# Kernel optimization log

Measured on AMD Instinct MI355X. Metric: run time of the kernel, lower is better.

## Reference

```python
import jax, jax.numpy as jnp
import numpy as np

B, T, C, H = 128, 512, 128, 64  # batch, seq, n_embd, head_size


def setup_inputs() -> dict:
    key = jax.random.key(0)
    ks = jax.random.split(key, 6)
    s = 1.0 / np.sqrt(C)
    return {
        "x": jax.random.normal(ks[0], (B, T, C), dtype=jnp.float32),
        "Wg": jax.random.normal(ks[1], (C, C), dtype=jnp.float32) * s,
        "bg": jnp.zeros((C,), dtype=jnp.float32),
        "Wk": jax.random.normal(ks[2], (C, H), dtype=jnp.float32) * s,
        "Wq": jax.random.normal(ks[3], (C, H), dtype=jnp.float32) * s,
        "Wv": jax.random.normal(ks[4], (C, H), dtype=jnp.float32) * s,
    }


def reference(x, Wg, bg, Wk, Wq, Wv):
    # GateLayer: x * sigmoid(Linear(x))
    g = jax.nn.sigmoid(jnp.einsum('btc,cd->btd', x, Wg) + bg)
    xg = x * g
    k = jnp.einsum('btc,ch->bth', xg, Wk)
    q = jnp.einsum('btc,ch->bth', xg, Wq)
    v = jnp.einsum('btc,ch->bth', xg, Wv)
    # NOTE: original scales by C**-0.5 (n_embd), not head_size**-0.5
    scale = C ** -0.5
    wei = jnp.einsum('bqh,bkh->bqk', q, k) * scale  # [B,T,T]
    causal = jnp.tril(jnp.ones((T, T), dtype=bool))
    wei = jnp.where(causal, wei, -jnp.inf)
    wei = jax.nn.softmax(wei, axis=-1)
    # dropout is identity in eval mode
    out = jnp.einsum('bqk,bkh->bqh', wei, v)  # [B,T,H]
    return out
```

## Files before the change

kernel.cpp:

```cpp
#include <hip/hip_runtime.h>


#define BB 128
#define TB 512
#define CC 128
#define HH 64

static constexpr float SCALE = 0.088388347648318447f;

typedef __attribute__((ext_vector_type(8))) short bf16x8;
typedef __attribute__((ext_vector_type(8))) unsigned short u16x8;
typedef __attribute__((ext_vector_type(4))) float f32x4;

__device__ inline unsigned short f2bf(float f) {
    union { float f; unsigned u; } x; x.f = f;
    unsigned r = x.u + 0x7fff + ((x.u >> 16) & 1);
    return (unsigned short)(r >> 16);
}
__device__ inline float bf2f(unsigned short h) {
    union { unsigned u; float f; } x; x.u = ((unsigned)h) << 16;
    return x.f;
}

__global__ void prep_weights(const float* __restrict__ Wg, const float* __restrict__ Wk,
                             const float* __restrict__ Wq, const float* __restrict__ Wv,
                             unsigned short* __restrict__ WgT, unsigned short* __restrict__ WkT,
                             unsigned short* __restrict__ WqT, unsigned short* __restrict__ WvT)
{
    int idx = blockIdx.x * 256 + threadIdx.x;
    if (idx < 16384) {
        int n = idx >> 7, k = idx & 127;
        WgT[idx] = f2bf(Wg[k * CC + n]);
    } else {
        int j = idx - 16384;
        int mtx = j >> 13;
        int r = j & 8191;
        int n = r >> 7, k = r & 127;
        const float* W = (mtx == 0) ? Wk : (mtx == 1) ? Wq : Wv;
        unsigned short* WT = (mtx == 0) ? WkT : (mtx == 1) ? WqT : WvT;
        WT[r] = f2bf(W[k * HH + n]);
    }
}

__global__ __launch_bounds__(256, 3) void gate_qkv_kernel(
    const float* __restrict__ x, const float* __restrict__ bg,
    const unsigned short* __restrict__ WgT, const unsigned short* __restrict__ WkT,
    const unsigned short* __restrict__ WqT, const unsigned short* __restrict__ WvT,
    unsigned short* __restrict__ qo, unsigned short* __restrict__ ko,
    unsigned short* __restrict__ vto)
{
    __shared__ unsigned short xsb[128 * 136];

    const int tid  = threadIdx.x;
    const int wv   = tid >> 6;
    const int lane = tid & 63;
    const int l15  = lane & 15;
    const int quad = lane >> 4;
    const int R0   = blockIdx.x * 128;

#pragma unroll
    for (int it = 0; it < 16; ++it) {
        int fid = tid + 256 * it;
        int r = fid >> 5, c4 = fid & 31;
        float4 xv = *(const float4*)(x + (size_t)(R0 + r) * CC + c4 * 4);
        ushort4 h;
        h.x = f2bf(xv.x); h.y = f2bf(xv.y); h.z = f2bf(xv.z); h.w = f2bf(xv.w);
        *(ushort4*)(xsb + r * 136 + c4 * 4) = h;
    }
    __syncthreads();

    bf16x8 bx[2][4];
#pragma unroll
    for (int mt = 0; mt < 2; ++mt)
#pragma unroll
        for (int kc = 0; kc < 4; ++kc)
            bx[mt][kc] = *(const bf16x8*)(xsb + (32 * wv + 16 * mt + l15) * 136 +
                                          kc * 32 + quad * 8);

    f32x4 acc[8][2];
#pragma unroll
    for (int nt = 0; nt < 8; ++nt)
#pragma unroll
        for (int mt = 0; mt < 2; ++mt) acc[nt][mt] = (f32x4){0.f, 0.f, 0.f, 0.f};

#pragma unroll
    for (int nt = 0; nt < 8; ++nt) {
        bf16x8 aw[4];
#pragma unroll
        for (int kc = 0; kc < 4; ++kc)
            aw[kc] = *(const bf16x8*)(WgT + (16 * nt + l15) * CC + kc * 32 + quad * 8);
#pragma unroll
        for (int mt = 0; mt < 2; ++mt)
#pragma unroll
            for (int kc = 0; kc < 4; ++kc)
                acc[nt][mt] = __builtin_amdgcn_mfma_f32_16x16x32_bf16(
                    aw[kc], bx[mt][kc], acc[nt][mt], 0, 0, 0);
    }

#pragma unroll
    for (int nt = 0; nt < 8; ++nt) {
        float4 bgv = *(const float4*)(bg + 16 * nt + quad * 4);
#pragma unroll
        for (int mt = 0; mt < 2; ++mt) {
            int m = 32 * wv + 16 * mt + l15;
            unsigned short* p = xsb + m * 136 + 16 * nt + quad * 4;
            ushort4 xb = *(const ushort4*)p;
            float e0 = __expf(-(acc[nt][mt][0] + bgv.x));
            float e1 = __expf(-(acc[nt][mt][1] + bgv.y));
            float e2 = __expf(-(acc[nt][mt][2] + bgv.z));
            float e3 = __expf(-(acc[nt][mt][3] + bgv.w));
            ushort4 o;
            o.x = f2bf(bf2f(xb.x) * __builtin_amdgcn_rcpf(1.f + e0));
            o.y = f2bf(bf2f(xb.y) * __builtin_amdgcn_rcpf(1.f + e1));
            o.z = f2bf(bf2f(xb.z) * __builtin_amdgcn_rcpf(1.f + e2));
            o.w = f2bf(bf2f(xb.w) * __builtin_amdgcn_rcpf(1.f + e3));
            *(ushort4*)p = o;
        }
    }
    __syncthreads();

#pragma unroll
    for (int mt = 0; mt < 2; ++mt)
#pragma unroll
        for (int kc = 0; kc < 4; ++kc)
            bx[mt][kc] = *(const bf16x8*)(xsb + (32 * wv + 16 * mt + l15) * 136 +
                                          kc * 32 + quad * 8);

    const int b = R0 >> 9, t0 = R0 & 511;
    for (int pj = 0; pj < 3; ++pj) {
        const unsigned short* WT = (pj == 0) ? WkT : (pj == 1) ? WqT : WvT;
        f32x4 pacc[4][2];
#pragma unroll
        for (int nt = 0; nt < 4; ++nt)
#pragma unroll
            for (int mt = 0; mt < 2; ++mt) pacc[nt][mt] = (f32x4){0.f, 0.f, 0.f, 0.f};

#pragma unroll
        for (int nt = 0; nt < 4; ++nt) {
            bf16x8 aw[4];
#pragma unroll
            for (int kc = 0; kc < 4; ++kc)
                aw[kc] = *(const bf16x8*)(WT + (16 * nt + l15) * CC + kc * 32 + quad * 8);
#pragma unroll
            for (int mt = 0; mt < 2; ++mt)
#pragma unroll
                for (int kc = 0; kc < 4; ++kc)
                    pacc[nt][mt] = __builtin_amdgcn_mfma_f32_16x16x32_bf16(
                        aw[kc], bx[mt][kc], pacc[nt][mt], 0, 0, 0);
        }

        if (pj < 2) {
            unsigned short* O = (pj == 0) ? ko : qo;
#pragma unroll
            for (int nt = 0; nt < 4; ++nt)
#pragma unroll
                for (int mt = 0; mt < 2; ++mt) {
                    int m = 32 * wv + 16 * mt + l15;
                    ushort4 h;
                    h.x = f2bf(pacc[nt][mt][0]); h.y = f2bf(pacc[nt][mt][1]);
                    h.z = f2bf(pacc[nt][mt][2]); h.w = f2bf(pacc[nt][mt][3]);
                    *(ushort4*)(O + (size_t)(R0 + m) * HH + 16 * nt + quad * 4) = h;
                }
        } else {
#pragma unroll
            for (int nt = 0; nt < 4; ++nt)
#pragma unroll
                for (int mt = 0; mt < 2; ++mt) {
                    int m = 32 * wv + 16 * mt + l15;
                    unsigned short* dst =
                        vto + (size_t)b * (HH * TB) + (16 * nt + quad * 4) * TB + t0 + m;
#pragma unroll
                    for (int r = 0; r < 4; ++r)
                        dst[r * TB] = f2bf(pacc[nt][mt][r]);
                }
        }
    }
}

__global__ __launch_bounds__(256) void attn_kernel(
    const unsigned short* __restrict__ q, const unsigned short* __restrict__ k,
    const unsigned short* __restrict__ vt, float* __restrict__ out)
{
    __shared__ unsigned short ks[64 * 72];
    __shared__ unsigned short vs[64 * 72];
    __shared__ unsigned short ps[64 * 76];

    const int tid  = threadIdx.x;
    const int wave = tid >> 6;
    const int lane = tid & 63;
    const int l15  = lane & 15;
    const int quad = lane >> 4;
    const int pr   = blockIdx.x;
    const int b    = blockIdx.y;
    const size_t base = (size_t)b * TB * HH;
    const int qtA = pr;

    const int r0 = tid >> 3,          c80 = (tid & 7) * 8;
    const int r1 = (tid + 256) >> 3,  c81 = (tid & 7) * 8;

    bf16x8 kr0 = *(const bf16x8*)(k + base + (size_t)r0 * HH + c80);
    bf16x8 kr1 = *(const bf16x8*)(k + base + (size_t)r1 * HH + c81);
    bf16x8 vr0 = *(const bf16x8*)(vt + base + (size_t)r0 * TB + c80);
    bf16x8 vr1 = *(const bf16x8*)(vt + base + (size_t)r1 * TB + c81);

    int qt = qtA, q0 = qtA * 64;
    const unsigned short* qrow = q + base + (size_t)(q0 + 16 * wave + l15) * HH;
    bf16x8 aq0 = *(const bf16x8*)(qrow + quad * 8);
    bf16x8 aq1 = *(const bf16x8*)(qrow + 32 + quad * 8);

    f32x4 o4[4];
    float mrow[4], lrow[4];
#pragma unroll
    for (int nt = 0; nt < 4; ++nt) o4[nt] = (f32x4){0.f, 0.f, 0.f, 0.f};
#pragma unroll
    for (int r = 0; r < 4; ++r) { mrow[r] = -1e30f; lrow[r] = 0.f; }

    for (int it = 0; it < 9; ++it) {
        const int kt = (it <= qtA) ? it : it - qtA - 1;

        __syncthreads();
        *(bf16x8*)(ks + r0 * 72 + c80) = kr0;
        *(bf16x8*)(ks + r1 * 72 + c81) = kr1;
        *(bf16x8*)(vs + r0 * 72 + c80) = vr0;
        *(bf16x8*)(vs + r1 * 72 + c81) = vr1;
        __syncthreads();

        if (it < 8) {
            const int itn = it + 1;
            const int ktn = (itn <= qtA) ? itn : itn - qtA - 1;
            const int k0n = ktn * 64;
            kr0 = *(const bf16x8*)(k + base + (size_t)(k0n + r0) * HH + c80);
            kr1 = *(const bf16x8*)(k + base + (size_t)(k0n + r1) * HH + c81);
            vr0 = *(const bf16x8*)(vt + base + (size_t)r0 * TB + k0n + c80);
            vr1 = *(const bf16x8*)(vt + base + (size_t)r1 * TB + k0n + c81);
        }

        f32x4 s[4];
#pragma unroll
        for (int nt = 0; nt < 4; ++nt) {
            bf16x8 bk0 = *(const bf16x8*)(ks + (16 * nt + l15) * 72 + quad * 8);
            bf16x8 bk1 = *(const bf16x8*)(ks + (16 * nt + l15) * 72 + 32 + quad * 8);
            f32x4 z = (f32x4){0.f, 0.f, 0.f, 0.f};
            z = __builtin_amdgcn_mfma_f32_16x16x32_bf16(aq0, bk0, z, 0, 0, 0);
            z = __builtin_amdgcn_mfma_f32_16x16x32_bf16(aq1, bk1, z, 0, 0, 0);
            s[nt] = z;
        }

        const bool diag = (kt == qt);
        float mx[4];
#pragma unroll
        for (int r = 0; r < 4; ++r) mx[r] = -1e30f;
#pragma unroll
        for (int nt = 0; nt < 4; ++nt)
#pragma unroll
            for (int r = 0; r < 4; ++r) {
                float sv = s[nt][r] * SCALE;
                if (diag && (16 * nt + l15) > (16 * wave + quad * 4 + r)) sv = -1e30f;
                s[nt][r] = sv;
                mx[r] = fmaxf(mx[r], sv);
            }

#pragma unroll
        for (int r = 0; r < 4; ++r) {
            mx[r] = fmaxf(mx[r], __shfl_xor(mx[r], 1));
            mx[r] = fmaxf(mx[r], __shfl_xor(mx[r], 2));
            mx[r] = fmaxf(mx[r], __shfl_xor(mx[r], 4));
            mx[r] = fmaxf(mx[r], __shfl_xor(mx[r], 8));
        }
        float alpha[4], psum[4];
#pragma unroll
        for (int r = 0; r < 4; ++r) {
            float mn = fmaxf(mrow[r], mx[r]);
            alpha[r] = __expf(mrow[r] - mn);
            mrow[r] = mn;
            psum[r] = 0.f;
        }
#pragma unroll
        for (int nt = 0; nt < 4; ++nt)
#pragma unroll
            for (int r = 0; r < 4; ++r) {
                float e = __expf(s[nt][r] - mrow[r]);
                psum[r] += e;
                ps[(16 * wave + quad * 4 + r) * 76 + 16 * nt + l15] = f2bf(e);
            }
#pragma unroll
        for (int r = 0; r < 4; ++r) {
            psum[r] += __shfl_xor(psum[r], 1);
            psum[r] += __shfl_xor(psum[r], 2);
            psum[r] += __shfl_xor(psum[r], 4);
            psum[r] += __shfl_xor(psum[r], 8);
            lrow[r] = lrow[r] * alpha[r] + psum[r];
        }
#pragma unroll
        for (int nt = 0; nt < 4; ++nt)
#pragma unroll
            for (int r = 0; r < 4; ++r) o4[nt][r] *= alpha[r];

        bf16x8 ap0 = *(const bf16x8*)(ps + (16 * wave + l15) * 76 + quad * 8);
        bf16x8 ap1 = *(const bf16x8*)(ps + (16 * wave + l15) * 76 + 32 + quad * 8);
#pragma unroll
        for (int nt = 0; nt < 4; ++nt) {
            bf16x8 bv0 = *(const bf16x8*)(vs + (16 * nt + l15) * 72 + quad * 8);
            bf16x8 bv1 = *(const bf16x8*)(vs + (16 * nt + l15) * 72 + 32 + quad * 8);
            o4[nt] = __builtin_amdgcn_mfma_f32_16x16x32_bf16(ap0, bv0, o4[nt], 0, 0, 0);
            o4[nt] = __builtin_amdgcn_mfma_f32_16x16x32_bf16(ap1, bv1, o4[nt], 0, 0, 0);
        }

        if (kt == qt) {
            float inv[4];
#pragma unroll
            for (int r = 0; r < 4; ++r) inv[r] = __builtin_amdgcn_rcpf(lrow[r]);
#pragma unroll
            for (int nt = 0; nt < 4; ++nt)
#pragma unroll
                for (int r = 0; r < 4; ++r)
                    out[base + (size_t)(q0 + 16 * wave + quad * 4 + r) * HH + 16 * nt + l15] =
                        o4[nt][r] * inv[r];
            if (it < 8) {
                qt = 7 - pr; q0 = qt * 64;
                const unsigned short* qrow2 = q + base + (size_t)(q0 + 16 * wave + l15) * HH;
                aq0 = *(const bf16x8*)(qrow2 + quad * 8);
                aq1 = *(const bf16x8*)(qrow2 + 32 + quad * 8);
#pragma unroll
                for (int nt = 0; nt < 4; ++nt) o4[nt] = (f32x4){0.f, 0.f, 0.f, 0.f};
#pragma unroll
                for (int r = 0; r < 4; ++r) { mrow[r] = -1e30f; lrow[r] = 0.f; }
            }
        }
    }
}

extern "C" void kernel_launch(void* const* d_in, const int* in_sizes, int n_in,
                              void* d_out, int out_size, void* d_ws, size_t ws_size,
                              hipStream_t stream) {
    const float* x  = (const float*)d_in[0];
    const float* Wg = (const float*)d_in[1];
    const float* bg = (const float*)d_in[2];
    const float* Wk = (const float*)d_in[3];
    const float* Wq = (const float*)d_in[4];
    const float* Wv = (const float*)d_in[5];
    float* out = (float*)d_out;

    unsigned short* ws = (unsigned short*)d_ws;
    const size_t BTH = (size_t)BB * TB * HH;
    unsigned short* qo  = ws;
    unsigned short* ko  = ws + BTH;
    unsigned short* vto = ws + 2 * BTH;
    unsigned short* WgT = ws + 3 * BTH;
    unsigned short* WkT = WgT + 16384;
    unsigned short* WqT = WkT + 8192;
    unsigned short* WvT = WqT + 8192;

    hipLaunchKernelGGL(prep_weights, dim3(160), dim3(256), 0, stream,
                       Wg, Wk, Wq, Wv, WgT, WkT, WqT, WvT);
    hipLaunchKernelGGL(gate_qkv_kernel, dim3(BB * TB / 128), dim3(256), 0, stream,
                       x, bg, WgT, WkT, WqT, WvT, qo, ko, vto);
    hipLaunchKernelGGL(attn_kernel, dim3(4, BB), dim3(256), 0, stream,
                       qo, ko, vto, out);
}
```

Measured before the change: 133.4 us.

## Share K/V tile loads across paired query tiles and prefetch weight fragments

The attention kernel now processes both paired query tiles (pr and 7-pr) at the same time. Each K/V tile is staged into shared memory once and used by both tiles, instead of the earlier sequential pass that reloaded the low tile's K/V range. The gate/QKV kernel double-buffers the weight fragment loads so the next n-tile's weights are fetched while the current MFMAs run, and the projection loop is fully unrolled. Launch bounds drop to 2 blocks per CU to give room for the extra registers from the dual accumulators, which risks lower occupancy.

```diff
diff --git a/kernel.cpp b/kernel.cpp
--- a/kernel.cpp
+++ b/kernel.cpp
@@ -42,7 +42,7 @@
     }
 }
 
-__global__ __launch_bounds__(256, 3) void gate_qkv_kernel(
+__global__ __launch_bounds__(256, 2) void gate_qkv_kernel(
     const float* __restrict__ x, const float* __restrict__ bg,
     const unsigned short* __restrict__ WgT, const unsigned short* __restrict__ WkT,
     const unsigned short* __restrict__ WqT, const unsigned short* __restrict__ WvT,
@@ -83,18 +83,30 @@
 #pragma unroll
         for (int mt = 0; mt < 2; ++mt) acc[nt][mt] = (f32x4){0.f, 0.f, 0.f, 0.f};
 
+    bf16x8 awA[4], awB[4];
+#pragma unroll
+    for (int kc = 0; kc < 4; ++kc)
+        awA[kc] = *(const bf16x8*)(WgT + l15 * CC + kc * 32 + quad * 8);
+
 #pragma unroll
     for (int nt = 0; nt < 8; ++nt) {
-        bf16x8 aw[4];
-#pragma unroll
-        for (int kc = 0; kc < 4; ++kc)
-            aw[kc] = *(const bf16x8*)(WgT + (16 * nt + l15) * CC + kc * 32 + quad * 8);
+        if (nt < 7) {
+#pragma unroll
+            for (int kc = 0; kc < 4; ++kc)
+                awB[kc] = *(const bf16x8*)(WgT + (16 * (nt + 1) + l15) * CC + kc * 32 + quad * 8);
+        } else {
+#pragma unroll
+            for (int kc = 0; kc < 4; ++kc)
+                awB[kc] = *(const bf16x8*)(WkT + l15 * CC + kc * 32 + quad * 8);
+        }
 #pragma unroll
         for (int mt = 0; mt < 2; ++mt)
 #pragma unroll
             for (int kc = 0; kc < 4; ++kc)
                 acc[nt][mt] = __builtin_amdgcn_mfma_f32_16x16x32_bf16(
-                    aw[kc], bx[mt][kc], acc[nt][mt], 0, 0, 0);
+                    awA[kc], bx[mt][kc], acc[nt][mt], 0, 0, 0);
+#pragma unroll
+        for (int kc = 0; kc < 4; ++kc) awA[kc] = awB[kc];
     }
 
 #pragma unroll
@@ -127,8 +139,8 @@
                                           kc * 32 + quad * 8);
 
     const int b = R0 >> 9, t0 = R0 & 511;
+#pragma unroll
     for (int pj = 0; pj < 3; ++pj) {
-        const unsigned short* WT = (pj == 0) ? WkT : (pj == 1) ? WqT : WvT;
         f32x4 pacc[4][2];
 #pragma unroll
         for (int nt = 0; nt < 4; ++nt)
@@ -137,16 +149,23 @@
 
 #pragma unroll
         for (int nt = 0; nt < 4; ++nt) {
-            bf16x8 aw[4];
-#pragma unroll
-            for (int kc = 0; kc < 4; ++kc)
-                aw[kc] = *(const bf16x8*)(WT + (16 * nt + l15) * CC + kc * 32 + quad * 8);
+            if (!(pj == 2 && nt == 3)) {
+                const unsigned short* Wcur = (pj == 0) ? WkT : (pj == 1) ? WqT : WvT;
+                const unsigned short* Wnxt = (pj == 0) ? WqT : WvT;
+                const unsigned short* Wp   = (nt < 3) ? Wcur : Wnxt;
+                const int ntn = (nt < 3) ? nt + 1 : 0;
+#pragma unroll
+                for (int kc = 0; kc < 4; ++kc)
+                    awB[kc] = *(const bf16x8*)(Wp + (16 * ntn + l15) * CC + kc * 32 + quad * 8);
+            }
 #pragma unroll
             for (int mt = 0; mt < 2; ++mt)
 #pragma unroll
                 for (int kc = 0; kc < 4; ++kc)
                     pacc[nt][mt] = __builtin_amdgcn_mfma_f32_16x16x32_bf16(
-                        aw[kc], bx[mt][kc], pacc[nt][mt], 0, 0, 0);
+                        awA[kc], bx[mt][kc], pacc[nt][mt], 0, 0, 0);
+#pragma unroll
+            for (int kc = 0; kc < 4; ++kc) awA[kc] = awB[kc];
         }
 
         if (pj < 2) {
@@ -177,7 +196,81 @@
     }
 }
 
-__global__ __launch_bounds__(256) void attn_kernel(
+__device__ __forceinline__ void smax_pv(f32x4* s, float* mrow, float* lrow,
+                                        f32x4* o4, unsigned short* ps,
+                                        const unsigned short* vs,
+                                        int wave, int l15, int quad)
+{
+    float mx[4];
+#pragma unroll
+    for (int r = 0; r < 4; ++r) mx[r] = -1e30f;
+#pragma unroll
+    for (int nt = 0; nt < 4; ++nt)
+#pragma unroll
+        for (int r = 0; r < 4; ++r) mx[r] = fmaxf(mx[r], s[nt][r]);
+#pragma unroll
+    for (int r = 0; r < 4; ++r) {
+        mx[r] = fmaxf(mx[r], __shfl_xor(mx[r], 1));
+        mx[r] = fmaxf(mx[r], __shfl_xor(mx[r], 2));
+        mx[r] = fmaxf(mx[r], __shfl_xor(mx[r], 4));
+        mx[r] = fmaxf(mx[r], __shfl_xor(mx[r], 8));
+    }
+    float alpha[4], psum[4];
+#pragma unroll
+    for (int r = 0; r < 4; ++r) {
+        float mn = fmaxf(mrow[r], mx[r]);
+        alpha[r] = __expf(mrow[r] - mn);
+        mrow[r] = mn;
+        psum[r] = 0.f;
+    }
+#pragma unroll
+    for (int nt = 0; nt < 4; ++nt)
+#pragma unroll
+        for (int r = 0; r < 4; ++r) {
+            float e = __expf(s[nt][r] - mrow[r]);
+            psum[r] += e;
+            ps[(16 * wave + quad * 4 + r) * 76 + 16 * nt + l15] = f2bf(e);
+        }
+#pragma unroll
+    for (int r = 0; r < 4; ++r) {
+        psum[r] += __shfl_xor(psum[r], 1);
+        psum[r] += __shfl_xor(psum[r], 2);
+        psum[r] += __shfl_xor(psum[r], 4);
+        psum[r] += __shfl_xor(psum[r], 8);
+        lrow[r] = lrow[r] * alpha[r] + psum[r];
+    }
+#pragma unroll
+    for (int nt = 0; nt < 4; ++nt)
+#pragma unroll
+        for (int r = 0; r < 4; ++r) o4[nt][r] *= alpha[r];
+
+    bf16x8 ap0 = *(const bf16x8*)(ps + (16 * wave + l15) * 76 + quad * 8);
+    bf16x8 ap1 = *(const bf16x8*)(ps + (16 * wave + l15) * 76 + 32 + quad * 8);
+#pragma unroll
+    for (int nt = 0; nt < 4; ++nt) {
+        bf16x8 bv0 = *(const bf16x8*)(vs + (16 * nt + l15) * 72 + quad * 8);
+        bf16x8 bv1 = *(const bf16x8*)(vs + (16 * nt + l15) * 72 + 32 + quad * 8);
+        o4[nt] = __builtin_amdgcn_mfma_f32_16x16x32_bf16(ap0, bv0, o4[nt], 0, 0, 0);
+        o4[nt] = __builtin_amdgcn_mfma_f32_16x16x32_bf16(ap1, bv1, o4[nt], 0, 0, 0);
+    }
+}
+
+__device__ __forceinline__ void attn_epilogue(const f32x4* o4, const float* lrow,
+                                              float* out, size_t base, int q0,
+                                              int wave, int l15, int quad)
+{
+    float inv[4];
+#pragma unroll
+    for (int r = 0; r < 4; ++r) inv[r] = __builtin_amdgcn_rcpf(lrow[r]);
+#pragma unroll
+    for (int nt = 0; nt < 4; ++nt)
+#pragma unroll
+        for (int r = 0; r < 4; ++r)
+            out[base + (size_t)(q0 + 16 * wave + quad * 4 + r) * HH + 16 * nt + l15] =
+                o4[nt][r] * inv[r];
+}
+
+__global__ __launch_bounds__(256, 2) void attn_kernel(
     const unsigned short* __restrict__ q, const unsigned short* __restrict__ k,
     const unsigned short* __restrict__ vt, float* __restrict__ out)
 {
@@ -193,141 +286,100 @@
     const int pr   = blockIdx.x;
     const int b    = blockIdx.y;
     const size_t base = (size_t)b * TB * HH;
-    const int qtA = pr;
-
-    const int r0 = tid >> 3,          c80 = (tid & 7) * 8;
-    const int r1 = (tid + 256) >> 3,  c81 = (tid & 7) * 8;
-
-    bf16x8 kr0 = *(const bf16x8*)(k + base + (size_t)r0 * HH + c80);
-    bf16x8 kr1 = *(const bf16x8*)(k + base + (size_t)r1 * HH + c81);
-    bf16x8 vr0 = *(const bf16x8*)(vt + base + (size_t)r0 * TB + c80);
-    bf16x8 vr1 = *(const bf16x8*)(vt + base + (size_t)r1 * TB + c81);
-
-    int qt = qtA, q0 = qtA * 64;
-    const unsigned short* qrow = q + base + (size_t)(q0 + 16 * wave + l15) * HH;
-    bf16x8 aq0 = *(const bf16x8*)(qrow + quad * 8);
-    bf16x8 aq1 = *(const bf16x8*)(qrow + 32 + quad * 8);
-
-    f32x4 o4[4];
-    float mrow[4], lrow[4];
-#pragma unroll
-    for (int nt = 0; nt < 4; ++nt) o4[nt] = (f32x4){0.f, 0.f, 0.f, 0.f};
-#pragma unroll
-    for (int r = 0; r < 4; ++r) { mrow[r] = -1e30f; lrow[r] = 0.f; }
-
-    for (int it = 0; it < 9; ++it) {
-        const int kt = (it <= qtA) ? it : it - qtA - 1;
-
+
+    const int qtA = pr, qtB = 7 - pr;
+    const int q0A = qtA * 64, q0B = qtB * 64;
+
+    const int r0 = tid >> 3, c8 = (tid & 7) * 8;
+    const int r1 = r0 + 32;
+
+    bf16x8 kr0 = *(const bf16x8*)(k + base + (size_t)r0 * HH + c8);
+    bf16x8 kr1 = *(const bf16x8*)(k + base + (size_t)r1 * HH + c8);
+    bf16x8 vr0 = *(const bf16x8*)(vt + base + (size_t)r0 * TB + c8);
+    bf16x8 vr1 = *(const bf16x8*)(vt + base + (size_t)r1 * TB + c8);
+
+    const unsigned short* qrA = q + base + (size_t)(q0A + 16 * wave + l15) * HH;
+    const unsigned short* qrB = q + base + (size_t)(q0B + 16 * wave + l15) * HH;
+    bf16x8 aqA0 = *(const bf16x8*)(qrA + quad * 8);
+    bf16x8 aqA1 = *(const bf16x8*)(qrA + 32 + quad * 8);
+    bf16x8 aqB0 = *(const bf16x8*)(qrB + quad * 8);
+    bf16x8 aqB1 = *(const bf16x8*)(qrB + 32 + quad * 8);
+
+    f32x4 oA[4], oB[4];
+    float mA[4], lA[4], mB[4], lB[4];
+#pragma unroll
+    for (int nt = 0; nt < 4; ++nt) {
+        oA[nt] = (f32x4){0.f, 0.f, 0.f, 0.f};
+        oB[nt] = (f32x4){0.f, 0.f, 0.f, 0.f};
+    }
+#pragma unroll
+    for (int r = 0; r < 4; ++r) { mA[r] = -1e30f; lA[r] = 0.f; mB[r] = -1e30f; lB[r] = 0.f; }
+
+    const int nIt = qtB + 1;
+    for (int kt = 0; kt < nIt; ++kt) {
         __syncthreads();
-        *(bf16x8*)(ks + r0 * 72 + c80) = kr0;
-        *(bf16x8*)(ks + r1 * 72 + c81) = kr1;
-        *(bf16x8*)(vs + r0 * 72 + c80) = vr0;
-        *(bf16x8*)(vs + r1 * 72 + c81) = vr1;
+        *(bf16x8*)(ks + r0 * 72 + c8) = kr0;
+        *(bf16x8*)(ks + r1 * 72 + c8) = kr1;
+        *(bf16x8*)(vs + r0 * 72 + c8) = vr0;
+        *(bf16x8*)(vs + r1 * 72 + c8) = vr1;
         __syncthreads();
 
-        if (it < 8) {
-            const int itn = it + 1;
-            const int ktn = (itn <= qtA) ? itn : itn - qtA - 1;
-            const int k0n = ktn * 64;
-            kr0 = *(const bf16x8*)(k + base + (size_t)(k0n + r0) * HH + c80);
-            kr1 = *(const bf16x8*)(k + base + (size_t)(k0n + r1) * HH + c81);
-            vr0 = *(const bf16x8*)(vt + base + (size_t)r0 * TB + k0n + c80);
-            vr1 = *(const bf16x8*)(vt + base + (size_t)r1 * TB + k0n + c81);
-        }
-
-        f32x4 s[4];
+        if (kt + 1 < nIt) {
+            const int k0n = (kt + 1) * 64;
+            kr0 = *(const bf16x8*)(k + base + (size_t)(k0n + r0) * HH + c8);
+            kr1 = *(const bf16x8*)(k + base + (size_t)(k0n + r1) * HH + c8);
+            vr0 = *(const bf16x8*)(vt + base + (size_t)r0 * TB + k0n + c8);
+            vr1 = *(const bf16x8*)(vt + base + (size_t)r1 * TB + k0n + c8);
+        }
+
+        const bool actA = (kt <= qtA);
+
+        f32x4 sA[4], sB[4];
 #pragma unroll
         for (int nt = 0; nt < 4; ++nt) {
             bf16x8 bk0 = *(const bf16x8*)(ks + (16 * nt + l15) * 72 + quad * 8);
             bf16x8 bk1 = *(const bf16x8*)(ks + (16 * nt + l15) * 72 + 32 + quad * 8);
-            f32x4 z = (f32x4){0.f, 0.f, 0.f, 0.f};
-            z = __builtin_amdgcn_mfma_f32_16x16x32_bf16(aq0, bk0, z, 0, 0, 0);
-            z = __builtin_amdgcn_mfma_f32_16x16x32_bf16(aq1, bk1, z, 0, 0, 0);
-            s[nt] = z;
-        }
-
-        const bool diag = (kt == qt);
-        float mx[4];
-#pragma unroll
-        for (int r = 0; r < 4; ++r) mx[r] = -1e30f;
-#pragma unroll
-        for (int nt = 0; nt < 4; ++nt)
-#pragma unroll
-            for (int r = 0; r < 4; ++r) {
-                float sv = s[nt][r] * SCALE;
-                if (diag && (16 * nt + l15) > (16 * wave + quad * 4 + r)) sv = -1e30f;
-                s[nt][r] = sv;
-                mx[r] = fmaxf(mx[r], sv);
+            f32x4 zb = (f32x4){0.f, 0.f, 0.f, 0.f};
+            zb = __builtin_amdgcn_mfma_f32_16x16x32_bf16(aqB0, bk0, zb, 0, 0, 0);
+            zb = __builtin_amdgcn_mfma_f32_16x16x32_bf16(aqB1, bk1, zb, 0, 0, 0);
+            sB[nt] = zb;
+            if (actA) {
+                f32x4 za = (f32x4){0.f, 0.f, 0.f, 0.f};
+                za = __builtin_amdgcn_mfma_f32_16x16x32_bf16(aqA0, bk0, za, 0, 0, 0);
+                za = __builtin_amdgcn_mfma_f32_16x16x32_bf16(aqA1, bk1, za, 0, 0, 0);
+                sA[nt] = za;
             }
-
-#pragma unroll
-        for (int r = 0; r < 4; ++r) {
-            mx[r] = fmaxf(mx[r], __shfl_xor(mx[r], 1));
-            mx[r] = fmaxf(mx[r], __shfl_xor(mx[r], 2));
-            mx[r] = fmaxf(mx[r], __shfl_xor(mx[r], 4));
-            mx[r] = fmaxf(mx[r], __shfl_xor(mx[r], 8));
-        }
-        float alpha[4], psum[4];
-#pragma unroll
-        for (int r = 0; r < 4; ++r) {
-            float mn = fmaxf(mrow[r], mx[r]);
-            alpha[r] = __expf(mrow[r] - mn);
-            mrow[r] = mn;
-            psum[r] = 0.f;
-        }
-#pragma unroll
-        for (int nt = 0; nt < 4; ++nt)
-#pragma unroll
-            for (int r = 0; r < 4; ++r) {
-                float e = __expf(s[nt][r] - mrow[r]);
-                psum[r] += e;
-                ps[(16 * wave + quad * 4 + r) * 76 + 16 * nt + l15] = f2bf(e);
-            }
-#pragma unroll
-        for (int r = 0; r < 4; ++r) {
-            psum[r] += __shfl_xor(psum[r], 1);
-            psum[r] += __shfl_xor(psum[r], 2);
-            psum[r] += __shfl_xor(psum[r], 4);
-            psum[r] += __shfl_xor(psum[r], 8);
-            lrow[r] = lrow[r] * alpha[r] + psum[r];
-        }
-#pragma unroll
-        for (int nt = 0; nt < 4; ++nt)
-#pragma unroll
-            for (int r = 0; r < 4; ++r) o4[nt][r] *= alpha[r];
-
-        bf16x8 ap0 = *(const bf16x8*)(ps + (16 * wave + l15) * 76 + quad * 8);
-        bf16x8 ap1 = *(const bf16x8*)(ps + (16 * wave + l15) * 76 + 32 + quad * 8);
-#pragma unroll
-        for (int nt = 0; nt < 4; ++nt) {
-            bf16x8 bv0 = *(const bf16x8*)(vs + (16 * nt + l15) * 72 + quad * 8);
-            bf16x8 bv1 = *(const bf16x8*)(vs + (16 * nt + l15) * 72 + 32 + quad * 8);
-            o4[nt] = __builtin_amdgcn_mfma_f32_16x16x32_bf16(ap0, bv0, o4[nt], 0, 0, 0);
-            o4[nt] = __builtin_amdgcn_mfma_f32_16x16x32_bf16(ap1, bv1, o4[nt], 0, 0, 0);
-        }
-
-        if (kt == qt) {
-            float inv[4];
-#pragma unroll
-            for (int r = 0; r < 4; ++r) inv[r] = __builtin_amdgcn_rcpf(lrow[r]);
+        }
+
+        if (actA) {
+            const bool diagA = (kt == qtA);
 #pragma unroll
             for (int nt = 0; nt < 4; ++nt)
 #pragma unroll
-                for (int r = 0; r < 4; ++r)
-                    out[base + (size_t)(q0 + 16 * wave + quad * 4 + r) * HH + 16 * nt + l15] =
-                        o4[nt][r] * inv[r];
-            if (it < 8) {
-                qt = 7 - pr; q0 = qt * 64;
-                const unsigned short* qrow2 = q + base + (size_t)(q0 + 16 * wave + l15) * HH;
-                aq0 = *(const bf16x8*)(qrow2 + quad * 8);
-                aq1 = *(const bf16x8*)(qrow2 + 32 + quad * 8);
-#pragma unroll
-                for (int nt = 0; nt < 4; ++nt) o4[nt] = (f32x4){0.f, 0.f, 0.f, 0.f};
-#pragma unroll
-                for (int r = 0; r < 4; ++r) { mrow[r] = -1e30f; lrow[r] = 0.f; }
-            }
-        }
-    }
+                for (int r = 0; r < 4; ++r) {
+                    float sv = sA[nt][r] * SCALE;
+                    if (diagA && (16 * nt + l15) > (16 * wave + quad * 4 + r)) sv = -1e30f;
+                    sA[nt][r] = sv;
+                }
+            smax_pv(sA, mA, lA, oA, ps, vs, wave, l15, quad);
+            if (diagA) attn_epilogue(oA, lA, out, base, q0A, wave, l15, quad);
+        }
+
+        {
+            const bool diagB = (kt == qtB);
+#pragma unroll
+            for (int nt = 0; nt < 4; ++nt)
+#pragma unroll
+                for (int r = 0; r < 4; ++r) {
+                    float sv = sB[nt][r] * SCALE;
+                    if (diagB && (16 * nt + l15) > (16 * wave + quad * 4 + r)) sv = -1e30f;
+                    sB[nt][r] = sv;
+                }
+            smax_pv(sB, mB, lB, oB, ps, vs, wave, l15, quad);
+        }
+    }
+
+    attn_epilogue(oB, lB, out, base, q0B, wave, l15, quad);
 }
 
 extern "C" void kernel_launch(void* const* d_in, const int* in_sizes, int n_in,
```

Result: no change. 134.2 us (+0.6%).
